# Optimization experiments

Measured on AMD Instinct MI355X. Metric: run time of the kernel, lower is better.

Reference implementation:

```python
import jax, jax.numpy as jnp
import numpy as np
from jax import lax

D_MODEL = 1024
N_HEADS = 16
HEAD_DIM = D_MODEL // N_HEADS
B, S = 4, 2048
EPS = 1e-5


def setup_inputs() -> dict:
    key = jax.random.key(0)
    ks = jax.random.split(key, 8)
    sc = 1.0 / np.sqrt(D_MODEL)
    return {
        "x": jax.random.normal(ks[0], (B, S, D_MODEL), dtype=jnp.float32),
        "Wq": jax.random.normal(ks[1], (D_MODEL, D_MODEL), dtype=jnp.float32) * sc,
        "Wk": jax.random.normal(ks[2], (D_MODEL, D_MODEL), dtype=jnp.float32) * sc,
        "Wv": jax.random.normal(ks[3], (D_MODEL, D_MODEL), dtype=jnp.float32) * sc,
        "Wa": jax.random.normal(ks[4], (D_MODEL, N_HEADS), dtype=jnp.float32) * sc,
        "ba": jnp.zeros((N_HEADS,), dtype=jnp.float32),
        "Wb": jax.random.normal(ks[5], (D_MODEL, N_HEADS), dtype=jnp.float32) * sc,
        "bb": jnp.zeros((N_HEADS,), dtype=jnp.float32),
        "Wg": jax.random.normal(ks[6], (D_MODEL, D_MODEL), dtype=jnp.float32) * sc,
        "Wo": jax.random.normal(ks[7], (D_MODEL, D_MODEL), dtype=jnp.float32) * sc,
        "g_norm": jnp.ones((D_MODEL,), dtype=jnp.float32),
    }


def _l2_normalize(v, eps=1e-12):
    # F.normalize(dim=-1) in float32
    v32 = v.astype(jnp.float32)
    n = jnp.sqrt(jnp.sum(v32 * v32, axis=-1, keepdims=True))
    return (v32 / jnp.maximum(n, eps)).astype(v.dtype)


def _rmsnorm(x, w):
    x32 = x.astype(jnp.float32)
    rms = lax.rsqrt(jnp.mean(x32 * x32, axis=-1, keepdims=True) + EPS)
    return (x32 * rms).astype(x.dtype) * w


def reference(x, Wq, Wk, Wv, Wa, ba, Wb, bb, Wg, Wo, g_norm):
    batch, seq_len, d_model = x.shape
    H, hd = N_HEADS, HEAD_DIM
    residual_input = x

    # projections -> [B, S, H, hd]
    q = (x @ Wq).reshape(batch, seq_len, H, hd)
    k = (x @ Wk).reshape(batch, seq_len, H, hd)
    v = (x @ Wv).reshape(batch, seq_len, H, hd)
    q = _l2_normalize(q)
    k = _l2_normalize(k)

    alpha = jax.nn.sigmoid(x @ Wa + ba)  # [B, S, H]
    beta = jax.nn.sigmoid(x @ Wb + bb)   # [B, S, H]

    # time-major for scan: [S, B, H, ...]
    qt = jnp.moveaxis(q, 1, 0)
    kt = jnp.moveaxis(k, 1, 0)
    vt = jnp.moveaxis(v, 1, 0)
    at = jnp.moveaxis(alpha, 1, 0)
    bt = jnp.moveaxis(beta, 1, 0)

    state0 = jnp.zeros((batch, H, hd, hd), dtype=x.dtype)

    def step(state, inp):
        q_t, k_t, v_t, a_t, b_t = inp  # [B,H,hd], [B,H]
        pred = jnp.einsum('bhde,bhd->bhe', state, k_t)
        error = v_t - pred
        update = jnp.einsum('bhe,bhd->bhde', b_t[..., None] * error, k_t)
        state = a_t[..., None, None] * state + update
        out = jnp.einsum('bhde,bhd->bhe', state, q_t)
        return state, out

    _, ys = lax.scan(step, state0, (qt, kt, vt, at, bt))  # ys: [S,B,H,hd]
    y = jnp.moveaxis(ys, 0, 1).reshape(batch, seq_len, d_model)

    gate = jax.nn.silu(residual_input @ Wg)
    y = _rmsnorm(y, g_norm) * gate
    return y @ Wo


if __name__ == "__main__":
    out = reference(**setup_inputs())
    print(out.shape)
```

## Files before the change

### kernel.cpp

```cpp
#include <hip/hip_runtime.h>
#include <hip/hip_bf16.h>
#include <math.h>

typedef __attribute__((ext_vector_type(8))) short bf16x8s;
typedef __attribute__((ext_vector_type(4))) float f32x4;

#define SEQ 2048
#define NTOK 8192
#define NQKV 3200

static __device__ __forceinline__ float bf2f(unsigned short u) {
  union { unsigned int i; float f; } c; c.i = ((unsigned int)u) << 16; return c.f;
}
static __device__ __forceinline__ unsigned short f2bf(float f) {
  union { float f; unsigned int i; } c; c.f = f;
  unsigned int x = c.i;
  return (unsigned short)((x + 0x7FFFu + ((x >> 16) & 1u)) >> 16);
}

static __device__ __forceinline__ float red16(float x) {
  union { float f; int i; } c, d;
  c.f = x; d.i = __builtin_amdgcn_update_dpp(0, c.i, 0xB1, 0xF, 0xF, true); x += d.f;
  c.f = x; d.i = __builtin_amdgcn_update_dpp(0, c.i, 0x4E, 0xF, 0xF, true); x += d.f;
  c.f = x; d.i = __builtin_amdgcn_update_dpp(0, c.i, 0x141, 0xF, 0xF, true); x += d.f;
  c.f = x; d.i = __builtin_amdgcn_update_dpp(0, c.i, 0x140, 0xF, 0xF, true); x += d.f;
  return x;
}

__global__ __launch_bounds__(256) void castx_k(const float* __restrict__ in,
                                               unsigned short* __restrict__ out, int n4) {
  int i = blockIdx.x * 256 + threadIdx.x;
  if (i >= n4) return;
  float4 v = ((const float4*)in)[i];
  ushort4 o;
  o.x = f2bf(v.x); o.y = f2bf(v.y); o.z = f2bf(v.z); o.w = f2bf(v.w);
  ((ushort4*)out)[i] = o;
}

__global__ void transpose_k(const float* __restrict__ in,
                            unsigned short* __restrict__ out, int R, int C) {
  __shared__ unsigned short tile[32][33];
  int c0 = blockIdx.x * 32, r0 = blockIdx.y * 32;
  int tx = threadIdx.x, ty = threadIdx.y;
  for (int i = ty; i < 32; i += 8)
    tile[i][tx] = f2bf(in[(size_t)(r0 + i) * C + c0 + tx]);
  __syncthreads();
  for (int i = ty; i < 32; i += 8)
    out[(size_t)(c0 + i) * R + r0 + tx] = tile[tx][i];
}

__global__ void build_wabT(const float* __restrict__ Wa,
                           const float* __restrict__ Wb,
                           unsigned short* __restrict__ rows) {
  int i = blockIdx.x * 256 + threadIdx.x;
  int j = i >> 10, k = i & 1023;
  float v = 0.f;
  if (j < 16) v = Wa[k * 16 + j];
  else if (j < 32) v = Wb[k * 16 + (j - 16)];
  rows[(size_t)j * 1024 + k] = f2bf(v);
}

template<int MODE>
__global__ __launch_bounds__(256) void gemm_bt(const unsigned short* __restrict__ A,
                                               const unsigned short* __restrict__ Bt,
                                               void* __restrict__ Cv,
                                               int M, int N, int K,
                                               const float* __restrict__ ba,
                                               const float* __restrict__ bbp,
                                               float* __restrict__ alphaF,
                                               float* __restrict__ betaF) {
  __shared__ __align__(16) unsigned short As[128 * 32];
  __shared__ __align__(16) unsigned short Bs[128 * 32];
  int tiles_n = N >> 7;
  int tm = blockIdx.x / tiles_n, tn = blockIdx.x % tiles_n;
  int m0 = tm << 7, n0 = tn << 7;
  int tid = threadIdx.x;
  int wave = tid >> 6, lane = tid & 63;
  int wm = wave >> 1, wn = wave & 1;
  int r = lane & 15, qd = lane >> 4;
  int lr = lane >> 2, lc = lane & 3;

  f32x4 acc[4][4];
#pragma unroll
  for (int mi = 0; mi < 4; mi++)
#pragma unroll
    for (int ni = 0; ni < 4; ni++) acc[mi][ni] = (f32x4){0.f, 0.f, 0.f, 0.f};

  for (int k0 = 0; k0 < K; k0 += 32) {
#pragma unroll
    for (int gi = 0; gi < 2; ++gi) {
      int g = wave + gi * 4;
      int row = g * 16 + lr;
      const unsigned short* ga = A + (size_t)(m0 + row) * K + k0 + lc * 8;
      const unsigned short* gb = Bt + (size_t)(n0 + row) * K + k0 + lc * 8;
      __builtin_amdgcn_global_load_lds(
          (const __attribute__((address_space(1))) unsigned int*)ga,
          (__attribute__((address_space(3))) unsigned int*)(As + g * 512 + lane * 8),
          16, 0, 0);
      __builtin_amdgcn_global_load_lds(
          (const __attribute__((address_space(1))) unsigned int*)gb,
          (__attribute__((address_space(3))) unsigned int*)(Bs + g * 512 + lane * 8),
          16, 0, 0);
    }
    __syncthreads();
    bf16x8s af[4], bfr[4];
#pragma unroll
    for (int mi = 0; mi < 4; mi++)
      af[mi] = *(const bf16x8s*)&As[(wm * 64 + mi * 16 + r) * 32 + qd * 8];
#pragma unroll
    for (int ni = 0; ni < 4; ni++)
      bfr[ni] = *(const bf16x8s*)&Bs[(wn * 64 + ni * 16 + r) * 32 + qd * 8];
#pragma unroll
    for (int mi = 0; mi < 4; mi++)
#pragma unroll
      for (int ni = 0; ni < 4; ni++)
        acc[mi][ni] = __builtin_amdgcn_mfma_f32_16x16x32_bf16(af[mi], bfr[ni], acc[mi][ni], 0, 0, 0);
    __syncthreads();
  }

  bool qk = (MODE == 2) && (n0 < 2048);
#pragma unroll
  for (int mi = 0; mi < 4; mi++) {
    f32x4 sc = (f32x4){1.f, 1.f, 1.f, 1.f};
    if (qk) {
      f32x4 ss = acc[mi][0] * acc[mi][0] + acc[mi][1] * acc[mi][1]
               + acc[mi][2] * acc[mi][2] + acc[mi][3] * acc[mi][3];
#pragma unroll
      for (int cc = 0; cc < 4; cc++) {
        float s = red16(ss[cc]);
        sc[cc] = 1.f / fmaxf(sqrtf(s), 1e-12f);
      }
    }
#pragma unroll
    for (int ni = 0; ni < 4; ni++)
#pragma unroll
      for (int reg = 0; reg < 4; reg++) {
        int m = m0 + wm * 64 + mi * 16 + qd * 4 + reg;
        int n = n0 + wn * 64 + ni * 16 + r;
        float a = acc[mi][ni][reg];
        if (MODE == 0) ((unsigned short*)Cv)[(size_t)m * N + n] = f2bf(a);
        else if (MODE == 1) ((float*)Cv)[(size_t)m * N + n] = a;
        else {
          if (qk) a *= sc[reg];
          if (n < 3072) ((unsigned short*)Cv)[(size_t)m * 3072 + n] = f2bf(a);
          else if (n < 3104) {
            int j = n - 3072;
            float bias = (j < 16) ? ba[j] : bbp[j - 16];
            float s = 1.f / (1.f + expf(-(a + bias)));
            if (j < 16) alphaF[(size_t)m * 16 + j] = s;
            else        betaF[(size_t)m * 16 + (j - 16)] = s;
          }
        }
      }
  }
}

#define D_OFF_STHI 0
#define D_OFF_STLO 8192
#define D_OFF_K    16384
#define D_OFF_Q    24576
#define D_OFF_V    32768
#define D_OFF_KT   40960
#define D_OFF_MT   45056
#define D_OFF_GBF  53248
#define D_OFF_CTHI 57344
#define D_OFF_CTLO 67584
#define D_OFF_W    77824
#define D_OFF_U    86016
#define D_OFF_AB   102400
#define D_LDS_SIZE 104512

static __device__ __forceinline__ float rdlane(float v, int i) {
  return __int_as_float(__builtin_amdgcn_readlane(__float_as_int(v), i));
}

__global__ __launch_bounds__(512, 2) void dscan_k(const unsigned short* __restrict__ qkv,
                                                  const float* __restrict__ alphaF,
                                                  const float* __restrict__ betaF,
                                                  unsigned short* __restrict__ y) {
  extern __shared__ char smem[];
  const int bh = blockIdx.x;
  const int b = bh >> 4, h = bh & 15;
  const int tid = threadIdx.x, wid = tid >> 6, lane = tid & 63;
  const int r = lane & 15, qd = lane >> 4;

  float* abf = (float*)(smem + D_OFF_AB);

  auto stage_jobs = [&](int cn) {
    int buf = cn & 1;
    int tok0 = b * SEQ + cn * 32;
    int row = lane >> 3, s8 = lane & 7;
    int sx = ((s8 ^ (row & 7)) * 8);
    {
      int p = (wid < 4) ? wid : wid - 4;
      int colbase = (wid < 4) ? (1024 + h * 64) : (h * 64);
      int off = (wid < 4) ? D_OFF_K : D_OFF_Q;
      const unsigned short* src = qkv + (size_t)(tok0 + p * 8 + row) * 3072 + colbase + sx;
      unsigned short* dst = (unsigned short*)(smem + off + buf * 4096 + p * 1024) + lane * 8;
      __builtin_amdgcn_global_load_lds(
          (const __attribute__((address_space(1))) unsigned int*)src,
          (__attribute__((address_space(3))) unsigned int*)dst, 16, 0, 0);
    }
    if (wid < 4) {
      int p = wid;
      const unsigned short* src = qkv + (size_t)(tok0 + p * 8 + row) * 3072 + 2048 + h * 64 + sx;
      unsigned short* dst = (unsigned short*)(smem + D_OFF_V + buf * 4096 + p * 1024) + lane * 8;
      __builtin_amdgcn_global_load_lds(
          (const __attribute__((address_space(1))) unsigned int*)src,
          (__attribute__((address_space(3))) unsigned int*)dst, 16, 0, 0);
    }
  };

  auto ab_compute = [&](int cn) {
    int t = lane & 31;
    int tok = b * SEQ + cn * 32 + t;
    float av = alphaF[(size_t)tok * 16 + h];
    float bv = betaF[(size_t)tok * 16 + h];
    float p = av;
#pragma unroll
    for (int s = 1; s < 32; s <<= 1) {
      float o = __shfl_up(p, s, 32);
      if ((lane & 31) >= s) p *= o;
    }
    float ep = __shfl_up(p, 1, 32);
    if ((lane & 31) == 0) ep = 1.f;
    float* ap = abf + (cn & 3) * 132;
    if (lane < 32) {
      ap[0 + t] = ep;
      ap[32 + t] = p;
      ap[64 + t] = 1.0f / p;
      if (t == 31) ap[128] = p;
    } else {
      ap[96 + t] = bv;
    }
  };

  auto gram_do = [&](int cn) {
    if (wid < 3 || wid > 6) return;
    int buf = cn & 1;
    const char* Kn = smem + D_OFF_K + buf * 4096;
    const char* Qn = smem + D_OFF_Q + buf * 4096;
    const float* ap = abf + (cn & 3) * 132;
    bool kk = (wid <= 4);
    int g0 = (kk ? (wid - 3) : (wid - 5)) * 2;
#pragma unroll
    for (int j = 0; j < 2; ++j) {
      int g = g0 + j, gi = g >> 1, gt = g & 1;
      f32x4 acc = (f32x4){0.f, 0.f, 0.f, 0.f};
#pragma unroll
      for (int ks = 0; ks < 2; ++ks) {
        int o = ks * 64 + qd * 16;
        bf16x8s af = *(const bf16x8s*)(Kn + (gi * 16 + r) * 128 + (o ^ ((r & 7) << 4)));
        bf16x8s bf = kk
            ? *(const bf16x8s*)(Kn + (gt * 16 + r) * 128 + (o ^ ((r & 7) << 4)))
            : *(const bf16x8s*)(Qn + (gt * 16 + r) * 128 + (o ^ ((r & 7) << 4)));
        acc = __builtin_amdgcn_mfma_f32_16x16x32_bf16(af, bf, acc, 0, 0, 0);
      }
      int tl = gt * 16 + r;
      f32x4 ei4 = *(const f32x4*)&ap[64 + gi * 16 + qd * 4];
      if (kk) {
        float bt = ap[96 + tl], ept = ap[0 + tl];
        float* Mtp = (float*)(smem + D_OFF_MT + buf * 4096);
#pragma unroll
        for (int reg = 0; reg < 4; ++reg) {
          int i = gi * 16 + qd * 4 + reg;
          Mtp[i * 32 + tl] = (i < tl) ? bt * ept * ei4[reg] * acc[reg] : 0.f;
        }
      } else {
        float et = ap[32 + tl];
        unsigned short* Gp = (unsigned short*)(smem + D_OFF_GBF + buf * 2048);
#pragma unroll
        for (int reg = 0; reg < 4; ++reg) {
          int i = gi * 16 + qd * 4 + reg;
          float v = (i <= tl) ? et * ei4[reg] * acc[reg] : 0.f;
          Gp[tl * 32 + i] = f2bf(v);
        }
      }
    }
  };

  float sreg[8];
#pragma unroll
  for (int i = 0; i < 8; ++i) sreg[i] = 0.f;

  {
    uint4 z = (uint4){0u, 0u, 0u, 0u};
    *(uint4*)(smem + D_OFF_STHI + tid * 16) = z;
    *(uint4*)(smem + D_OFF_STLO + tid * 16) = z;
  }
  stage_jobs(0);
  if (wid == 0) ab_compute(0);
  else if (wid == 1) ab_compute(1);
  __syncthreads();
  gram_do(0);
  __syncthreads();

  const char* SThi = smem + D_OFF_STHI;
  const char* STlo = smem + D_OFF_STLO;

  for (int c = 0; c < 64; ++c) {
    const int cbuf = c & 1, cs = c & 3;
    if (c + 1 < 64) stage_jobs(c + 1);
    {
      int tt = wid >> 2, te = wid & 3;
      const char* Kc = smem + D_OFF_K + cbuf * 4096;
      f32x4 acc = (f32x4){0.f, 0.f, 0.f, 0.f};
#pragma unroll
      for (int ks = 0; ks < 2; ++ks) {
        int o = ks * 64 + qd * 16;
        bf16x8s af = *(const bf16x8s*)(Kc + (tt * 16 + r) * 128 + (o ^ ((r & 7) << 4)));
        bf16x8s bhv = *(const bf16x8s*)(SThi + (te * 16 + r) * 128 + (o ^ ((r & 7) << 4)));
        bf16x8s blv = *(const bf16x8s*)(STlo + (te * 16 + r) * 128 + (o ^ ((r & 7) << 4)));
        acc = __builtin_amdgcn_mfma_f32_16x16x32_bf16(af, bhv, acc, 0, 0, 0);
        acc = __builtin_amdgcn_mfma_f32_16x16x32_bf16(af, blv, acc, 0, 0, 0);
      }
      float* Wp = (float*)(smem + D_OFF_W);
#pragma unroll
      for (int reg = 0; reg < 4; ++reg)
        Wp[(tt * 16 + qd * 4 + reg) * 64 + te * 16 + r] = acc[reg];
    }
    if (c >= 1) {
      int cc = c - 1, buf = cc & 1;
      int ty = wid >> 2, te = wid & 3;
      const char* Gp = smem + D_OFF_GBF + buf * 2048;
      bf16x8s af = *(const bf16x8s*)(Gp + (ty * 16 + r) * 64 + qd * 16);
      bf16x8s bhv = *(const bf16x8s*)(smem + D_OFF_CTHI + buf * 5120 + (te * 16 + r) * 80 + qd * 16);
      bf16x8s blv = *(const bf16x8s*)(smem + D_OFF_CTLO + buf * 5120 + (te * 16 + r) * 80 + qd * 16);
      f32x4 acc = (f32x4){0.f, 0.f, 0.f, 0.f};
      acc = __builtin_amdgcn_mfma_f32_16x16x32_bf16(af, bhv, acc, 0, 0, 0);
      acc = __builtin_amdgcn_mfma_f32_16x16x32_bf16(af, blv, acc, 0, 0, 0);
      const float* Up = (const float*)(smem + D_OFF_U + buf * 8192);
      f32x4 e4 = *(const f32x4*)&abf[(cc & 3) * 132 + 32 + ty * 16 + qd * 4];
#pragma unroll
      for (int reg = 0; reg < 4; ++reg) {
        int t = ty * 16 + qd * 4 + reg, e = te * 16 + r;
        float yv = fmaf(e4[reg], Up[t * 64 + e], acc[reg]);
        y[(size_t)(b * SEQ + cc * 32 + t) * 1024 + h * 64 + e] = f2bf(yv);
      }
    }
    __syncthreads();

    if (wid == 0) {
      const float* Wp = (const float*)(smem + D_OFF_W);
      const char* Vb = smem + D_OFF_V + cbuf * 4096;
      const float* ap = abf + cs * 132;
      float vb = ap[96 + (lane & 31)];
      float vep = ap[0 + (lane & 31)];
      float d_[32], r_[32];
#pragma unroll
      for (int i = 0; i < 32; ++i) r_[i] = 0.f;
#pragma unroll
      for (int i = 0; i < 32; ++i) {
        float w = Wp[i * 64 + lane];
        unsigned short vx = *(const unsigned short*)(Vb + (i * 128 + ((lane * 2) ^ ((i & 7) << 4))));
        d_[i] = rdlane(vb, i) * fmaf(-rdlane(vep, i), w, bf2f(vx));
      }
      const float* Mtp = (const float*)(smem + D_OFF_MT + cbuf * 4096);
#pragma unroll
      for (int i = 0; i < 32; ++i) {
        float cv = d_[i] - r_[i];
        d_[i] = cv;
#pragma unroll
        for (int cb4 = 0; cb4 < 8; ++cb4) {
          if (cb4 * 4 + 3 > i) {
            f32x4 m4 = *(const f32x4*)&Mtp[i * 32 + cb4 * 4];
            r_[cb4 * 4 + 0] = fmaf(m4[0], cv, r_[cb4 * 4 + 0]);
            r_[cb4 * 4 + 1] = fmaf(m4[1], cv, r_[cb4 * 4 + 1]);
            r_[cb4 * 4 + 2] = fmaf(m4[2], cv, r_[cb4 * 4 + 2]);
            r_[cb4 * 4 + 3] = fmaf(m4[3], cv, r_[cb4 * 4 + 3]);
          }
        }
      }
      unsigned int ph[16], pl[16];
#pragma unroll
      for (int j = 0; j < 16; ++j) {
        unsigned short h0 = f2bf(d_[2 * j]), h1 = f2bf(d_[2 * j + 1]);
        ph[j] = (unsigned int)h0 | ((unsigned int)h1 << 16);
        float l0 = d_[2 * j] - bf2f(h0), l1 = d_[2 * j + 1] - bf2f(h1);
        pl[j] = (unsigned int)f2bf(l0) | ((unsigned int)f2bf(l1) << 16);
      }
      char* Ch = smem + D_OFF_CTHI + cbuf * 5120 + lane * 80;
      char* Cl = smem + D_OFF_CTLO + cbuf * 5120 + lane * 80;
#pragma unroll
      for (int k = 0; k < 4; ++k) {
        *(uint4*)(Ch + k * 16) = (uint4){ph[4 * k], ph[4 * k + 1], ph[4 * k + 2], ph[4 * k + 3]};
        *(uint4*)(Cl + k * 16) = (uint4){pl[4 * k], pl[4 * k + 1], pl[4 * k + 2], pl[4 * k + 3]};
      }
    } else {
      if (wid <= 4) {
        const char* Qc = smem + D_OFF_Q + cbuf * 4096;
        float* Up = (float*)(smem + D_OFF_U + cbuf * 8192);
#pragma unroll
        for (int j = 0; j < 2; ++j) {
          int u = (wid - 1) * 2 + j, tu = u >> 2, te = u & 3;
          f32x4 acc = (f32x4){0.f, 0.f, 0.f, 0.f};
#pragma unroll
          for (int ks = 0; ks < 2; ++ks) {
            int o = ks * 64 + qd * 16;
            bf16x8s af = *(const bf16x8s*)(Qc + (tu * 16 + r) * 128 + (o ^ ((r & 7) << 4)));
            bf16x8s bhv = *(const bf16x8s*)(SThi + (te * 16 + r) * 128 + (o ^ ((r & 7) << 4)));
            bf16x8s blv = *(const bf16x8s*)(STlo + (te * 16 + r) * 128 + (o ^ ((r & 7) << 4)));
            acc = __builtin_amdgcn_mfma_f32_16x16x32_bf16(af, bhv, acc, 0, 0, 0);
            acc = __builtin_amdgcn_mfma_f32_16x16x32_bf16(af, blv, acc, 0, 0, 0);
          }
#pragma unroll
          for (int reg = 0; reg < 4; ++reg)
            Up[(tu * 16 + qd * 4 + reg) * 64 + te * 16 + r] = acc[reg];
        }
      }
      if (c + 1 < 64) gram_do(c + 1);
      if (wid == 7) {
        const float* ap = abf + cs * 132;
        float vei = ap[64 + (lane & 31)];
        float e31 = ap[128];
        const char* Kc = smem + D_OFF_K + cbuf * 4096;
        unsigned short* KT = (unsigned short*)(smem + D_OFF_KT);
        unsigned int pk[16];
#pragma unroll
        for (int i = 0; i < 32; ++i) {
          unsigned short kv = *(const unsigned short*)(Kc + (i * 128 + ((lane * 2) ^ ((i & 7) << 4))));
          float f = bf2f(kv) * (e31 * rdlane(vei, i));
          unsigned short o = f2bf(f);
          if (i & 1) pk[i >> 1] |= ((unsigned int)o << 16);
          else       pk[i >> 1] = o;
        }
#pragma unroll
        for (int k = 0; k < 4; ++k)
          *(uint4*)((char*)KT + lane * 64 + k * 16) =
              (uint4){pk[4 * k], pk[4 * k + 1], pk[4 * k + 2], pk[4 * k + 3]};
      }
      if (wid == 2 && c + 2 < 64) ab_compute(c + 2);
    }
    __syncthreads();

    {
      float e31 = abf[cs * 132 + 128];
      const char* KT = smem + D_OFF_KT;
#pragma unroll
      for (int j = 0; j < 2; ++j) {
        int s = wid * 2 + j, td = s >> 2, te = s & 3;
        bf16x8s af = *(const bf16x8s*)(KT + (td * 16 + r) * 64 + qd * 16);
        bf16x8s bhv = *(const bf16x8s*)(smem + D_OFF_CTHI + cbuf * 5120 + (te * 16 + r) * 80 + qd * 16);
        bf16x8s blv = *(const bf16x8s*)(smem + D_OFF_CTLO + cbuf * 5120 + (te * 16 + r) * 80 + qd * 16);
        f32x4 acc = (f32x4){0.f, 0.f, 0.f, 0.f};
        acc = __builtin_amdgcn_mfma_f32_16x16x32_bf16(af, bhv, acc, 0, 0, 0);
        acc = __builtin_amdgcn_mfma_f32_16x16x32_bf16(af, blv, acc, 0, 0, 0);
#pragma unroll
        for (int reg = 0; reg < 4; ++reg) {
          int d = td * 16 + qd * 4 + reg, e = te * 16 + r;
          float sv = fmaf(e31, sreg[j * 4 + reg], acc[reg]);
          sreg[j * 4 + reg] = sv;
          unsigned short hi = f2bf(sv);
          float lo = sv - bf2f(hi);
          *(unsigned short*)(smem + D_OFF_STHI + e * 128 + ((d * 2) ^ ((e & 7) << 4))) = hi;
          *(unsigned short*)(smem + D_OFF_STLO + e * 128 + ((d * 2) ^ ((e & 7) << 4))) = f2bf(lo);
        }
      }
    }
    __syncthreads();
  }

  {
    int cc = 63, buf = cc & 1;
    int ty = wid >> 2, te = wid & 3;
    const char* Gp = smem + D_OFF_GBF + buf * 2048;
    bf16x8s af = *(const bf16x8s*)(Gp + (ty * 16 + r) * 64 + qd * 16);
    bf16x8s bhv = *(const bf16x8s*)(smem + D_OFF_CTHI + buf * 5120 + (te * 16 + r) * 80 + qd * 16);
    bf16x8s blv = *(const bf16x8s*)(smem + D_OFF_CTLO + buf * 5120 + (te * 16 + r) * 80 + qd * 16);
    f32x4 acc = (f32x4){0.f, 0.f, 0.f, 0.f};
    acc = __builtin_amdgcn_mfma_f32_16x16x32_bf16(af, bhv, acc, 0, 0, 0);
    acc = __builtin_amdgcn_mfma_f32_16x16x32_bf16(af, blv, acc, 0, 0, 0);
    const float* Up = (const float*)(smem + D_OFF_U + buf * 8192);
    f32x4 e4 = *(const f32x4*)&abf[(cc & 3) * 132 + 32 + ty * 16 + qd * 4];
#pragma unroll
    for (int reg = 0; reg < 4; ++reg) {
      int t = ty * 16 + qd * 4 + reg, e = te * 16 + r;
      float yv = fmaf(e4[reg], Up[t * 64 + e], acc[reg]);
      y[(size_t)(b * SEQ + cc * 32 + t) * 1024 + h * 64 + e] = f2bf(yv);
    }
  }
}

__global__ __launch_bounds__(256) void rmsgate_k(const unsigned short* __restrict__ y,
                                                 const unsigned short* __restrict__ gl,
                                                 const float* __restrict__ gnorm,
                                                 unsigned short* __restrict__ z) {
  __shared__ float red[4];
  int row = blockIdx.x, tid = threadIdx.x;
  size_t base = (size_t)row * 1024 + tid * 4;
  uint2 yv = *(const uint2*)&y[base];
  float f0 = bf2f((unsigned short)(yv.x & 0xffff)), f1 = bf2f((unsigned short)(yv.x >> 16));
  float f2 = bf2f((unsigned short)(yv.y & 0xffff)), f3 = bf2f((unsigned short)(yv.y >> 16));
  float ss = f0 * f0 + f1 * f1 + f2 * f2 + f3 * f3;
#pragma unroll
  for (int s = 1; s < 64; s <<= 1) ss += __shfl_xor(ss, s);
  if ((tid & 63) == 0) red[tid >> 6] = ss;
  __syncthreads();
  ss = red[0] + red[1] + red[2] + red[3];
  float rms = rsqrtf(ss * (1.0f / 1024.0f) + 1e-5f);
  uint2 gv = *(const uint2*)&gl[base];
  float4 gn = *(const float4*)&gnorm[tid * 4];
  float g[4] = {bf2f((unsigned short)(gv.x & 0xffff)), bf2f((unsigned short)(gv.x >> 16)),
                bf2f((unsigned short)(gv.y & 0xffff)), bf2f((unsigned short)(gv.y >> 16))};
  float gnv[4] = {gn.x, gn.y, gn.z, gn.w};
  float fv[4] = {f0, f1, f2, f3};
  unsigned short o[4];
#pragma unroll
  for (int jj = 0; jj < 4; jj++) {
    float gate = g[jj] / (1.f + expf(-g[jj]));
    o[jj] = f2bf(fv[jj] * rms * gnv[jj] * gate);
  }
  uint2 ov;
  ov.x = (unsigned int)o[0] | ((unsigned int)o[1] << 16);
  ov.y = (unsigned int)o[2] | ((unsigned int)o[3] << 16);
  *(uint2*)&z[base] = ov;
}

extern "C" void kernel_launch(void* const* d_in, const int* in_sizes, int n_in,
                              void* d_out, int out_size, void* d_ws, size_t ws_size,
                              hipStream_t stream) {
  const float* x     = (const float*)d_in[0];
  const float* Wq    = (const float*)d_in[1];
  const float* Wk    = (const float*)d_in[2];
  const float* Wv    = (const float*)d_in[3];
  const float* Wa    = (const float*)d_in[4];
  const float* ba    = (const float*)d_in[5];
  const float* Wb    = (const float*)d_in[6];
  const float* bb    = (const float*)d_in[7];
  const float* Wg    = (const float*)d_in[8];
  const float* Wo    = (const float*)d_in[9];
  const float* gnorm = (const float*)d_in[10];
  float* out = (float*)d_out;

  unsigned short* xbf    = (unsigned short*)d_ws;
  unsigned short* Bt_qkv = xbf + (size_t)NTOK * 1024;
  unsigned short* Bt_g   = Bt_qkv + (size_t)NQKV * 1024;
  unsigned short* Bt_o   = Bt_g + (size_t)1024 * 1024;
  unsigned short* qkv    = Bt_o + (size_t)1024 * 1024;
  unsigned short* gatelin= qkv + (size_t)NTOK * 3072;
  unsigned short* ybuf   = gatelin + (size_t)NTOK * 1024;
  float* alphaF          = (float*)(ybuf + (size_t)NTOK * 1024);
  float* betaF           = alphaF + (size_t)NTOK * 16;
  unsigned short* zbuf   = xbf;

  static int dscan_inited = 0;
  if (!dscan_inited) {
    hipFuncSetAttribute((const void*)dscan_k,
                        hipFuncAttributeMaxDynamicSharedMemorySize, D_LDS_SIZE);
    dscan_inited = 1;
  }

  castx_k<<<NTOK * 1024 / 4 / 256, 256, 0, stream>>>(x, xbf, NTOK * 1024 / 4);
  dim3 tb(32, 8);
  transpose_k<<<dim3(32, 32), tb, 0, stream>>>(Wq, Bt_qkv, 1024, 1024);
  transpose_k<<<dim3(32, 32), tb, 0, stream>>>(Wk, Bt_qkv + (size_t)1024 * 1024, 1024, 1024);
  transpose_k<<<dim3(32, 32), tb, 0, stream>>>(Wv, Bt_qkv + (size_t)2048 * 1024, 1024, 1024);
  transpose_k<<<dim3(32, 32), tb, 0, stream>>>(Wg, Bt_g, 1024, 1024);
  transpose_k<<<dim3(32, 32), tb, 0, stream>>>(Wo, Bt_o, 1024, 1024);
  build_wabT<<<512, 256, 0, stream>>>(Wa, Wb, Bt_qkv + (size_t)3072 * 1024);

  gemm_bt<2><<<(NTOK / 128) * (NQKV / 128), 256, 0, stream>>>(
      xbf, Bt_qkv, qkv, NTOK, NQKV, 1024, ba, bb, alphaF, betaF);
  gemm_bt<0><<<(NTOK / 128) * (1024 / 128), 256, 0, stream>>>(
      xbf, Bt_g, gatelin, NTOK, 1024, 1024, nullptr, nullptr, nullptr, nullptr);
  dscan_k<<<64, 512, D_LDS_SIZE, stream>>>(qkv, alphaF, betaF, ybuf);
  rmsgate_k<<<NTOK, 256, 0, stream>>>(ybuf, gatelin, gnorm, zbuf);
  gemm_bt<1><<<(NTOK / 128) * (1024 / 128), 256, 0, stream>>>(
      zbuf, Bt_o, out, NTOK, 1024, 1024, nullptr, nullptr, nullptr, nullptr);
}
```

Measured before the change: 538.3 us.

## Split chunked delta-rule scan into parallel prep, serial combine, and parallel output kernels

Replaces the single 64-block sequential scan kernel with three kernels. The first computes per-chunk intra-chunk quantities (WY-style corrections, gram matrices, scaled keys) across 4096 blocks. The second does only the serial inter-chunk state recurrence and writes state snapshots. The third computes outputs in parallel across 2048 blocks. The aim is to move most work off the 64-block critical path, at the cost of large workspace traffic and extra launches. The path is gated on workspace size, and a gram_do prefetch call is also added to the old scan loop.

```diff
diff --git a/kernel.cpp b/kernel.cpp
--- a/kernel.cpp
+++ b/kernel.cpp
@@ -8,6 +8,7 @@
 #define SEQ 2048
 #define NTOK 8192
 #define NQKV 3200
+#define NUNIT 4096
 
 static __device__ __forceinline__ float bf2f(unsigned short u) {
   union { unsigned int i; float f; } c; c.i = ((unsigned int)u) << 16; return c.f;
@@ -26,6 +27,17 @@
   c.f = x; d.i = __builtin_amdgcn_update_dpp(0, c.i, 0x140, 0xF, 0xF, true); x += d.f;
   return x;
 }
+
+static __device__ __forceinline__ float rdlane(float v, int i) {
+  return __int_as_float(__builtin_amdgcn_readlane(__float_as_int(v), i));
+}
+
+#define GLD16(SRC, DST) __builtin_amdgcn_global_load_lds( \
+    (const __attribute__((address_space(1))) unsigned int*)(SRC), \
+    (__attribute__((address_space(3))) unsigned int*)(DST), 16, 0, 0)
+#define GLD4(SRC, DST) __builtin_amdgcn_global_load_lds( \
+    (const __attribute__((address_space(1))) unsigned int*)(SRC), \
+    (__attribute__((address_space(3))) unsigned int*)(DST), 4, 0, 0)
 
 __global__ __launch_bounds__(256) void castx_k(const float* __restrict__ in,
                                                unsigned short* __restrict__ out, int n4) {
@@ -93,14 +105,8 @@
       int row = g * 16 + lr;
       const unsigned short* ga = A + (size_t)(m0 + row) * K + k0 + lc * 8;
       const unsigned short* gb = Bt + (size_t)(n0 + row) * K + k0 + lc * 8;
-      __builtin_amdgcn_global_load_lds(
-          (const __attribute__((address_space(1))) unsigned int*)ga,
-          (__attribute__((address_space(3))) unsigned int*)(As + g * 512 + lane * 8),
-          16, 0, 0);
-      __builtin_amdgcn_global_load_lds(
-          (const __attribute__((address_space(1))) unsigned int*)gb,
-          (__attribute__((address_space(3))) unsigned int*)(Bs + g * 512 + lane * 8),
-          16, 0, 0);
+      GLD16(ga, As + g * 512 + lane * 8);
+      GLD16(gb, Bs + g * 512 + lane * 8);
     }
     __syncthreads();
     bf16x8s af[4], bfr[4];
@@ -170,10 +176,6 @@
 #define D_OFF_AB   102400
 #define D_LDS_SIZE 104512
 
-static __device__ __forceinline__ float rdlane(float v, int i) {
-  return __int_as_float(__builtin_amdgcn_readlane(__float_as_int(v), i));
-}
-
 __global__ __launch_bounds__(512, 2) void dscan_k(const unsigned short* __restrict__ qkv,
                                                   const float* __restrict__ alphaF,
                                                   const float* __restrict__ betaF,
@@ -197,17 +199,13 @@
       int off = (wid < 4) ? D_OFF_K : D_OFF_Q;
       const unsigned short* src = qkv + (size_t)(tok0 + p * 8 + row) * 3072 + colbase + sx;
       unsigned short* dst = (unsigned short*)(smem + off + buf * 4096 + p * 1024) + lane * 8;
-      __builtin_amdgcn_global_load_lds(
-          (const __attribute__((address_space(1))) unsigned int*)src,
-          (__attribute__((address_space(3))) unsigned int*)dst, 16, 0, 0);
+      GLD16(src, dst);
     }
     if (wid < 4) {
       int p = wid;
       const unsigned short* src = qkv + (size_t)(tok0 + p * 8 + row) * 3072 + 2048 + h * 64 + sx;
       unsigned short* dst = (unsigned short*)(smem + D_OFF_V + buf * 4096 + p * 1024) + lane * 8;
-      __builtin_amdgcn_global_load_lds(
-          (const __attribute__((address_space(1))) unsigned int*)src,
-          (__attribute__((address_space(3))) unsigned int*)dst, 16, 0, 0);
+      GLD16(src, dst);
     }
   };
 
@@ -457,6 +455,7 @@
         }
       }
     }
+    if (c + 1 < 64) gram_do(c + 1);
     __syncthreads();
   }
 
@@ -477,6 +476,454 @@
       int t = ty * 16 + qd * 4 + reg, e = te * 16 + r;
       float yv = fmaf(e4[reg], Up[t * 64 + e], acc[reg]);
       y[(size_t)(b * SEQ + cc * 32 + t) * 1024 + h * 64 + e] = f2bf(yv);
+    }
+  }
+}
+
+#define AK   0
+#define AQ   4096
+#define AV   8192
+#define AMT  12288
+#define AGS  16896
+#define AKP  19456
+#define AAB  24576
+#define ASZ  25120
+
+__global__ __launch_bounds__(256) void aprep_k(const unsigned short* __restrict__ qkv,
+                                               const float* __restrict__ alphaF,
+                                               const float* __restrict__ betaF,
+                                               unsigned char* __restrict__ RbHi,
+                                               unsigned char* __restrict__ RbLo,
+                                               unsigned char* __restrict__ Kpg,
+                                               unsigned char* __restrict__ Gg,
+                                               float* __restrict__ wg,
+                                               float* __restrict__ eing) {
+  __shared__ __align__(16) char smA[ASZ];
+  const int u = blockIdx.x;
+  const int bh = u >> 6, c = u & 63;
+  const int b = bh >> 4, h = bh & 15;
+  const int tid = threadIdx.x, wid = tid >> 6, lane = tid & 63;
+  const int r = lane & 15, qd = lane >> 4;
+  float* ab = (float*)(smA + AAB);
+
+  {
+    int tok0 = b * SEQ + c * 32;
+    int row = lane >> 3, s8 = lane & 7;
+    int sx = ((s8 ^ (row & 7)) * 8);
+    const unsigned short* base = qkv + (size_t)(tok0 + wid * 8 + row) * 3072 + h * 64 + sx;
+    GLD16(base + 1024, smA + AK + wid * 1024 + lane * 16);
+    GLD16(base,        smA + AQ + wid * 1024 + lane * 16);
+    GLD16(base + 2048, smA + AV + wid * 1024 + lane * 16);
+  }
+  if (wid == 0) {
+    int t = lane & 31;
+    int tok = b * SEQ + c * 32 + t;
+    float av = alphaF[(size_t)tok * 16 + h];
+    float bv = betaF[(size_t)tok * 16 + h];
+    float p = av;
+#pragma unroll
+    for (int s = 1; s < 32; s <<= 1) {
+      float o = __shfl_up(p, s, 32);
+      if ((lane & 31) >= s) p *= o;
+    }
+    float ep = __shfl_up(p, 1, 32);
+    if ((lane & 31) == 0) ep = 1.f;
+    if (lane < 32) {
+      ab[0 + t] = ep;
+      ab[32 + t] = p;
+      ab[64 + t] = 1.0f / p;
+      if (t == 31) ab[128] = p;
+    } else {
+      ab[96 + t] = bv;
+    }
+  }
+  __syncthreads();
+
+  const int sw = ((r & 7) << 4);
+  if (wid < 2) {
+    int gi = wid;
+    float* Mtp = (float*)(smA + AMT);
+    f32x4 ei4 = *(const f32x4*)&ab[64 + gi * 16 + qd * 4];
+#pragma unroll
+    for (int gt = 0; gt < 2; ++gt) {
+      f32x4 acc = (f32x4){0.f, 0.f, 0.f, 0.f};
+#pragma unroll
+      for (int ks = 0; ks < 2; ++ks) {
+        int o = ks * 64 + qd * 16;
+        bf16x8s af = *(const bf16x8s*)(smA + AK + (gi * 16 + r) * 128 + (o ^ sw));
+        bf16x8s bf = *(const bf16x8s*)(smA + AK + (gt * 16 + r) * 128 + (o ^ sw));
+        acc = __builtin_amdgcn_mfma_f32_16x16x32_bf16(af, bf, acc, 0, 0, 0);
+      }
+      int tl = gt * 16 + r;
+      float bep = ab[96 + tl] * ab[0 + tl];
+#pragma unroll
+      for (int reg = 0; reg < 4; ++reg) {
+        int i = gi * 16 + qd * 4 + reg;
+        Mtp[i * 36 + tl] = (i < tl) ? bep * ei4[reg] * acc[reg] : 0.f;
+      }
+    }
+  } else {
+    int gi = wid - 2;
+    unsigned short* Gp = (unsigned short*)(smA + AGS);
+    f32x4 ei4 = *(const f32x4*)&ab[64 + gi * 16 + qd * 4];
+#pragma unroll
+    for (int gt = 0; gt < 2; ++gt) {
+      f32x4 acc = (f32x4){0.f, 0.f, 0.f, 0.f};
+#pragma unroll
+      for (int ks = 0; ks < 2; ++ks) {
+        int o = ks * 64 + qd * 16;
+        bf16x8s af = *(const bf16x8s*)(smA + AK + (gi * 16 + r) * 128 + (o ^ sw));
+        bf16x8s bf = *(const bf16x8s*)(smA + AQ + (gt * 16 + r) * 128 + (o ^ sw));
+        acc = __builtin_amdgcn_mfma_f32_16x16x32_bf16(af, bf, acc, 0, 0, 0);
+      }
+      int tl = gt * 16 + r;
+      float et = ab[32 + tl];
+#pragma unroll
+      for (int reg = 0; reg < 4; ++reg) {
+        int i = gi * 16 + qd * 4 + reg;
+        float v = (i <= tl) ? et * ei4[reg] * acc[reg] : 0.f;
+        Gp[tl * 40 + i] = f2bf(v);
+      }
+    }
+    {
+      int i0 = (wid - 2) * 16;
+      float e31 = ab[128];
+#pragma unroll
+      for (int ii = 0; ii < 16; ++ii) {
+        int i = i0 + ii;
+        unsigned short kv = *(const unsigned short*)(smA + AK + i * 128 + ((lane * 2) ^ ((i & 7) << 4)));
+        float f = bf2f(kv) * (e31 * ab[64 + i]);
+        *(unsigned short*)(smA + AKP + lane * 64 + ((i * 2) ^ ((lane & 3) << 4))) = f2bf(f);
+      }
+    }
+  }
+  __syncthreads();
+
+  if (wid < 2) {
+    float d_[32], r_[32];
+#pragma unroll
+    for (int i = 0; i < 32; ++i) r_[i] = 0.f;
+#pragma unroll
+    for (int i = 0; i < 32; ++i) {
+      unsigned short xv;
+      if (wid == 0) xv = *(const unsigned short*)(smA + AK + i * 128 + ((lane * 2) ^ ((i & 7) << 4)));
+      else          xv = *(const unsigned short*)(smA + AV + i * 128 + ((lane * 2) ^ ((i & 7) << 4)));
+      float scv = (wid == 0) ? ab[96 + i] * ab[0 + i] : ab[96 + i];
+      d_[i] = scv * bf2f(xv);
+    }
+    const float* Mtp = (const float*)(smA + AMT);
+#pragma unroll
+    for (int i = 0; i < 32; ++i) {
+      float cv = d_[i] - r_[i];
+      d_[i] = cv;
+#pragma unroll
+      for (int cb4 = 0; cb4 < 8; ++cb4) {
+        if (cb4 * 4 + 3 > i) {
+          f32x4 m4 = *(const f32x4*)&Mtp[i * 36 + cb4 * 4];
+          r_[cb4 * 4 + 0] = fmaf(m4[0], cv, r_[cb4 * 4 + 0]);
+          r_[cb4 * 4 + 1] = fmaf(m4[1], cv, r_[cb4 * 4 + 1]);
+          r_[cb4 * 4 + 2] = fmaf(m4[2], cv, r_[cb4 * 4 + 2]);
+          r_[cb4 * 4 + 3] = fmaf(m4[3], cv, r_[cb4 * 4 + 3]);
+        }
+      }
+    }
+    if (wid == 0) {
+      size_t ub = (size_t)u * 4096;
+#pragma unroll
+      for (int t = 0; t < 32; ++t) {
+        unsigned short hi = f2bf(d_[t]);
+        float lo = d_[t] - bf2f(hi);
+        int off = t * 128 + ((lane * 2) ^ ((t & 7) << 4));
+        *(unsigned short*)(RbHi + ub + off) = hi;
+        *(unsigned short*)(RbLo + ub + off) = f2bf(lo);
+      }
+    } else {
+      float* wp = wg + (size_t)u * 2048;
+#pragma unroll
+      for (int t = 0; t < 32; ++t) wp[t * 64 + lane] = d_[t];
+    }
+  } else if (wid == 2) {
+    const char* s = smA + AGS + lane * 40;
+    unsigned char* dG = Gg + (size_t)u * 2560 + lane * 40;
+#pragma unroll
+    for (int k2 = 0; k2 < 5; ++k2)
+      *(uint2*)(dG + k2 * 8) = *(const uint2*)(s + k2 * 8);
+    if (lane < 32) eing[(size_t)u * 64 + lane] = ab[32 + lane];
+    if (lane == 32) eing[(size_t)u * 64 + 32] = ab[128];
+  } else {
+    const char* s = smA + AKP;
+    unsigned char* dK = Kpg + (size_t)u * 4096;
+#pragma unroll
+    for (int k2 = 0; k2 < 4; ++k2)
+      *(uint4*)(dK + lane * 64 + k2 * 16) = *(const uint4*)(s + lane * 64 + k2 * 16);
+  }
+}
+
+#define BSH  0
+#define BSL  8192
+#define BRH  16384
+#define BRL  24576
+#define BKP  32768
+#define BW   40960
+#define BCTH 57344
+#define BCTL 61440
+#define BSZ  65536
+
+__global__ __launch_bounds__(256) void bcomb_k(const unsigned char* __restrict__ RbHi,
+                                               const unsigned char* __restrict__ RbLo,
+                                               const unsigned char* __restrict__ Kpg,
+                                               float* __restrict__ wcg,
+                                               const float* __restrict__ eing,
+                                               unsigned char* __restrict__ Sing) {
+  extern __shared__ char smB[];
+  const int bh = blockIdx.x;
+  const int u_base = bh * 64;
+  const int tid = threadIdx.x, wid = tid >> 6, lane = tid & 63;
+  const int r = lane & 15, qd = lane >> 4;
+  const int sw7 = ((r & 7) << 4), sw3 = ((r & 3) << 4);
+
+  auto stageB = [&](int cn, int buf) {
+    int u = u_base + cn;
+    for (int j = wid; j < 20; j += 4) {
+      const unsigned char* src; char* dst;
+      if (j < 4)       { src = RbHi + (size_t)u * 4096 + j * 1024;       dst = smB + BRH + buf * 4096 + j * 1024; }
+      else if (j < 8)  { src = RbLo + (size_t)u * 4096 + (j - 4) * 1024; dst = smB + BRL + buf * 4096 + (j - 4) * 1024; }
+      else if (j < 12) { src = Kpg + (size_t)u * 4096 + (j - 8) * 1024;  dst = smB + BKP + buf * 4096 + (j - 8) * 1024; }
+      else             { src = (const unsigned char*)wcg + (size_t)u * 8192 + (j - 12) * 1024;
+                         dst = smB + BW + buf * 8192 + (j - 12) * 1024; }
+      GLD16(src + lane * 16, dst + lane * 16);
+    }
+  };
+
+#pragma unroll
+  for (int k = 0; k < 4; ++k)
+    *(uint4*)(smB + tid * 64 + k * 16) = (uint4){0u, 0u, 0u, 0u};
+  float sreg[16];
+#pragma unroll
+  for (int i = 0; i < 16; ++i) sreg[i] = 0.f;
+
+  stageB(0, 0);
+  float e31c = eing[(size_t)u_base * 64 + 32];
+  __syncthreads();
+
+  for (int c = 0; c < 64; ++c) {
+    const int buf = c & 1;
+    const int u = u_base + c;
+    float e31n = 0.f;
+    if (c + 1 < 64) {
+      stageB(c + 1, buf ^ 1);
+      e31n = eing[(size_t)(u + 1) * 64 + 32];
+    }
+    if (!(c & 1)) {
+#pragma unroll
+      for (int k = 0; k < 4; ++k)
+        *(uint4*)(Sing + (size_t)(u >> 1) * 16384 + k * 4096 + tid * 16) =
+            *(const uint4*)(smB + k * 4096 + tid * 16);
+    }
+    f32x4 accP[2];
+#pragma unroll
+    for (int tt = 0; tt < 2; ++tt) {
+      accP[tt] = (f32x4){0.f, 0.f, 0.f, 0.f};
+#pragma unroll
+      for (int ks = 0; ks < 2; ++ks) {
+        int o = ks * 64 + qd * 16;
+        bf16x8s sh = *(const bf16x8s*)(smB + BSH + (wid * 16 + r) * 128 + (o ^ sw7));
+        bf16x8s sl = *(const bf16x8s*)(smB + BSL + (wid * 16 + r) * 128 + (o ^ sw7));
+        bf16x8s rh = *(const bf16x8s*)(smB + BRH + buf * 4096 + (tt * 16 + r) * 128 + (o ^ sw7));
+        bf16x8s rl = *(const bf16x8s*)(smB + BRL + buf * 4096 + (tt * 16 + r) * 128 + (o ^ sw7));
+        accP[tt] = __builtin_amdgcn_mfma_f32_16x16x32_bf16(rh, sh, accP[tt], 0, 0, 0);
+        accP[tt] = __builtin_amdgcn_mfma_f32_16x16x32_bf16(rh, sl, accP[tt], 0, 0, 0);
+        accP[tt] = __builtin_amdgcn_mfma_f32_16x16x32_bf16(rl, sh, accP[tt], 0, 0, 0);
+      }
+    }
+    {
+      const float* wp = (const float*)(smB + BW + buf * 8192);
+#pragma unroll
+      for (int tt = 0; tt < 2; ++tt)
+#pragma unroll
+        for (int reg = 0; reg < 4; ++reg) {
+          int t = tt * 16 + qd * 4 + reg, e = wid * 16 + r;
+          float cv = wp[t * 64 + e] - accP[tt][reg];
+          unsigned short hi = f2bf(cv);
+          int off = e * 64 + ((t * 2) ^ ((e & 3) << 4));
+          *(unsigned short*)(smB + BCTH + off) = hi;
+          *(unsigned short*)(smB + BCTL + off) = f2bf(cv - bf2f(hi));
+        }
+    }
+    __syncthreads();
+    *(uint4*)((unsigned char*)wcg + (size_t)u * 8192 + tid * 16) =
+        *(const uint4*)(smB + BCTH + tid * 16);
+    *(uint4*)((unsigned char*)wcg + (size_t)u * 8192 + 4096 + tid * 16) =
+        *(const uint4*)(smB + BCTL + tid * 16);
+#pragma unroll
+    for (int j = 0; j < 4; ++j) {
+      f32x4 acc = (f32x4){0.f, 0.f, 0.f, 0.f};
+      bf16x8s af = *(const bf16x8s*)(smB + BKP + buf * 4096 + (wid * 16 + r) * 64 + ((qd * 16) ^ sw3));
+      bf16x8s ch = *(const bf16x8s*)(smB + BCTH + (j * 16 + r) * 64 + ((qd * 16) ^ sw3));
+      bf16x8s cl = *(const bf16x8s*)(smB + BCTL + (j * 16 + r) * 64 + ((qd * 16) ^ sw3));
+      acc = __builtin_amdgcn_mfma_f32_16x16x32_bf16(af, ch, acc, 0, 0, 0);
+      acc = __builtin_amdgcn_mfma_f32_16x16x32_bf16(af, cl, acc, 0, 0, 0);
+#pragma unroll
+      for (int reg = 0; reg < 4; ++reg) {
+        int d = wid * 16 + qd * 4 + reg, e = j * 16 + r;
+        float sv = fmaf(e31c, sreg[j * 4 + reg], acc[reg]);
+        sreg[j * 4 + reg] = sv;
+        unsigned short hi = f2bf(sv);
+        int off = e * 128 + ((d * 2) ^ ((e & 7) << 4));
+        *(unsigned short*)(smB + BSH + off) = hi;
+        *(unsigned short*)(smB + BSL + off) = f2bf(sv - bf2f(hi));
+      }
+    }
+    e31c = e31n;
+    __syncthreads();
+  }
+}
+
+#define XSH  0
+#define XSL  8192
+#define XQ   16384
+#define XC   24576
+#define XG   40960
+#define XKP  46080
+#define XSZ  50176
+
+__global__ __launch_bounds__(256) void cout2_k(const unsigned short* __restrict__ qkv,
+                                               const float* __restrict__ wcg,
+                                               const unsigned char* __restrict__ Gg,
+                                               const unsigned char* __restrict__ Kpg,
+                                               const float* __restrict__ eing,
+                                               const unsigned char* __restrict__ Sing,
+                                               unsigned short* __restrict__ y) {
+  __shared__ __align__(16) char smC[XSZ];
+  const int p = blockIdx.x;
+  const int bh = p >> 5, pr = p & 31;
+  const int b = bh >> 4, h = bh & 15;
+  const int u0 = bh * 64 + pr * 2;
+  const int tid = threadIdx.x, wid = tid >> 6, lane = tid & 63;
+  const int r = lane & 15, qd = lane >> 4;
+  const int sw7 = ((r & 7) << 4), sw3 = ((r & 3) << 4);
+  const int tok0 = b * SEQ + pr * 64;
+
+  for (int j = wid; j < 44; j += 4) {
+    if (j < 16) {
+      GLD16(Sing + (size_t)(u0 >> 1) * 16384 + j * 1024 + lane * 16,
+            smC + XSH + j * 1024 + lane * 16);
+    } else if (j < 24) {
+      int q = (j - 16) >> 2, pt = (j - 16) & 3;
+      int row = lane >> 3, s8 = lane & 7;
+      int sx = ((s8 ^ (row & 7)) * 8);
+      const unsigned short* src = qkv + (size_t)(tok0 + q * 32 + pt * 8 + row) * 3072 + h * 64 + sx;
+      GLD16(src, smC + XQ + q * 4096 + pt * 1024 + lane * 16);
+    } else if (j < 40) {
+      int q = (j - 24) >> 3, pt = (j - 24) & 7;
+      GLD16((const unsigned char*)wcg + (size_t)(u0 + q) * 8192 + pt * 1024 + lane * 16,
+            smC + XC + q * 8192 + pt * 1024 + lane * 16);
+    } else {
+      GLD16(Kpg + (size_t)u0 * 4096 + (j - 40) * 1024 + lane * 16,
+            smC + XKP + (j - 40) * 1024 + lane * 16);
+    }
+  }
+  if (wid < 2) {
+    const unsigned char* src = Gg + (size_t)(u0 + wid) * 2560;
+    char* dst = smC + XG + wid * 2560;
+    GLD16(src + lane * 16, dst + lane * 16);
+    GLD16(src + 1024 + lane * 16, dst + 1024 + lane * 16);
+    GLD4(src + 2048 + lane * 4, dst + 2048 + lane * 4);
+    GLD4(src + 2304 + lane * 4, dst + 2304 + lane * 4);
+  }
+  __syncthreads();
+
+  f32x4 accS[4];
+#pragma unroll
+  for (int half = 0; half < 1; ++half) {
+    f32x4 accU[2], accG[2];
+#pragma unroll
+    for (int tt = 0; tt < 2; ++tt) {
+      accU[tt] = (f32x4){0.f, 0.f, 0.f, 0.f};
+#pragma unroll
+      for (int ks = 0; ks < 2; ++ks) {
+        int o = ks * 64 + qd * 16;
+        bf16x8s sh = *(const bf16x8s*)(smC + XSH + (wid * 16 + r) * 128 + (o ^ sw7));
+        bf16x8s sl = *(const bf16x8s*)(smC + XSL + (wid * 16 + r) * 128 + (o ^ sw7));
+        bf16x8s qa = *(const bf16x8s*)(smC + XQ + (tt * 16 + r) * 128 + (o ^ sw7));
+        accU[tt] = __builtin_amdgcn_mfma_f32_16x16x32_bf16(qa, sh, accU[tt], 0, 0, 0);
+        accU[tt] = __builtin_amdgcn_mfma_f32_16x16x32_bf16(qa, sl, accU[tt], 0, 0, 0);
+      }
+      bf16x8s ga = *(const bf16x8s*)(smC + XG + (tt * 16 + r) * 80 + qd * 16);
+      bf16x8s ch = *(const bf16x8s*)(smC + XC + (wid * 16 + r) * 64 + ((qd * 16) ^ sw3));
+      bf16x8s cl = *(const bf16x8s*)(smC + XC + 4096 + (wid * 16 + r) * 64 + ((qd * 16) ^ sw3));
+      accG[tt] = (f32x4){0.f, 0.f, 0.f, 0.f};
+      accG[tt] = __builtin_amdgcn_mfma_f32_16x16x32_bf16(ga, ch, accG[tt], 0, 0, 0);
+      accG[tt] = __builtin_amdgcn_mfma_f32_16x16x32_bf16(ga, cl, accG[tt], 0, 0, 0);
+    }
+#pragma unroll
+    for (int tt = 0; tt < 2; ++tt) {
+      f32x4 e4 = *(const f32x4*)&eing[(size_t)u0 * 64 + tt * 16 + qd * 4];
+#pragma unroll
+      for (int reg = 0; reg < 4; ++reg) {
+        int t = tt * 16 + qd * 4 + reg, e = wid * 16 + r;
+        y[(size_t)(tok0 + t) * 1024 + h * 64 + e] =
+            f2bf(fmaf(e4[reg], accU[tt][reg], accG[tt][reg]));
+      }
+    }
+#pragma unroll
+    for (int j = 0; j < 4; ++j) {
+      accS[j] = (f32x4){0.f, 0.f, 0.f, 0.f};
+      bf16x8s af = *(const bf16x8s*)(smC + XKP + (wid * 16 + r) * 64 + ((qd * 16) ^ sw3));
+      bf16x8s ch = *(const bf16x8s*)(smC + XC + (j * 16 + r) * 64 + ((qd * 16) ^ sw3));
+      bf16x8s cl = *(const bf16x8s*)(smC + XC + 4096 + (j * 16 + r) * 64 + ((qd * 16) ^ sw3));
+      accS[j] = __builtin_amdgcn_mfma_f32_16x16x32_bf16(af, ch, accS[j], 0, 0, 0);
+      accS[j] = __builtin_amdgcn_mfma_f32_16x16x32_bf16(af, cl, accS[j], 0, 0, 0);
+    }
+  }
+  __syncthreads();
+  {
+    float e31 = eing[(size_t)u0 * 64 + 32];
+#pragma unroll
+    for (int j = 0; j < 4; ++j)
+#pragma unroll
+      for (int reg = 0; reg < 4; ++reg) {
+        int d = wid * 16 + qd * 4 + reg, e = j * 16 + r;
+        int off = e * 128 + ((d * 2) ^ ((e & 7) << 4));
+        float sA = bf2f(*(const unsigned short*)(smC + XSH + off)) +
+                   bf2f(*(const unsigned short*)(smC + XSL + off));
+        float sv = fmaf(e31, sA, accS[j][reg]);
+        unsigned short hi = f2bf(sv);
+        *(unsigned short*)(smC + XSH + off) = hi;
+        *(unsigned short*)(smC + XSL + off) = f2bf(sv - bf2f(hi));
+      }
+  }
+  __syncthreads();
+  {
+    f32x4 accU[2], accG[2];
+#pragma unroll
+    for (int tt = 0; tt < 2; ++tt) {
+      accU[tt] = (f32x4){0.f, 0.f, 0.f, 0.f};
+#pragma unroll
+      for (int ks = 0; ks < 2; ++ks) {
+        int o = ks * 64 + qd * 16;
+        bf16x8s sh = *(const bf16x8s*)(smC + XSH + (wid * 16 + r) * 128 + (o ^ sw7));
+        bf16x8s sl = *(const bf16x8s*)(smC + XSL + (wid * 16 + r) * 128 + (o ^ sw7));
+        bf16x8s qa = *(const bf16x8s*)(smC + XQ + 4096 + (tt * 16 + r) * 128 + (o ^ sw7));
+        accU[tt] = __builtin_amdgcn_mfma_f32_16x16x32_bf16(qa, sh, accU[tt], 0, 0, 0);
+        accU[tt] = __builtin_amdgcn_mfma_f32_16x16x32_bf16(qa, sl, accU[tt], 0, 0, 0);
+      }
+      bf16x8s ga = *(const bf16x8s*)(smC + XG + 2560 + (tt * 16 + r) * 80 + qd * 16);
+      bf16x8s ch = *(const bf16x8s*)(smC + XC + 8192 + (wid * 16 + r) * 64 + ((qd * 16) ^ sw3));
+      bf16x8s cl = *(const bf16x8s*)(smC + XC + 8192 + 4096 + (wid * 16 + r) * 64 + ((qd * 16) ^ sw3));
+      accG[tt] = (f32x4){0.f, 0.f, 0.f, 0.f};
+      accG[tt] = __builtin_amdgcn_mfma_f32_16x16x32_bf16(ga, ch, accG[tt], 0, 0, 0);
+      accG[tt] = __builtin_amdgcn_mfma_f32_16x16x32_bf16(ga, cl, accG[tt], 0, 0, 0);
+    }
+#pragma unroll
+    for (int tt = 0; tt < 2; ++tt) {
+      f32x4 e4 = *(const f32x4*)&eing[(size_t)(u0 + 1) * 64 + tt * 16 + qd * 4];
+#pragma unroll
+      for (int reg = 0; reg < 4; ++reg) {
+        int t = tt * 16 + qd * 4 + reg, e = wid * 16 + r;
+        y[(size_t)(tok0 + 32 + t) * 1024 + h * 64 + e] =
+            f2bf(fmaf(e4[reg], accU[tt][reg], accG[tt][reg]));
+      }
     }
   }
 }
@@ -543,11 +990,23 @@
   float* betaF           = alphaF + (size_t)NTOK * 16;
   unsigned short* zbuf   = xbf;
 
-  static int dscan_inited = 0;
-  if (!dscan_inited) {
+  unsigned char* RbHi = (unsigned char*)xbf;
+  unsigned char* RbLo = (unsigned char*)ybuf;
+  float* eing         = (float*)Bt_qkv;
+  unsigned char* Kpg  = (unsigned char*)(betaF + (size_t)NTOK * 16);
+  unsigned char* Gg   = Kpg + (size_t)NUNIT * 4096;
+  float* wcg          = (float*)(Gg + (size_t)NUNIT * 2560);
+  unsigned char* Sing = (unsigned char*)wcg + (size_t)NUNIT * 8192;
+  const unsigned long long need_new = 206831616ull;
+  const bool use_new = (ws_size >= need_new);
+
+  static int inited = 0;
+  if (!inited) {
     hipFuncSetAttribute((const void*)dscan_k,
                         hipFuncAttributeMaxDynamicSharedMemorySize, D_LDS_SIZE);
-    dscan_inited = 1;
+    hipFuncSetAttribute((const void*)bcomb_k,
+                        hipFuncAttributeMaxDynamicSharedMemorySize, BSZ);
+    inited = 1;
   }
 
   castx_k<<<NTOK * 1024 / 4 / 256, 256, 0, stream>>>(x, xbf, NTOK * 1024 / 4);
@@ -563,7 +1022,15 @@
       xbf, Bt_qkv, qkv, NTOK, NQKV, 1024, ba, bb, alphaF, betaF);
   gemm_bt<0><<<(NTOK / 128) * (1024 / 128), 256, 0, stream>>>(
       xbf, Bt_g, gatelin, NTOK, 1024, 1024, nullptr, nullptr, nullptr, nullptr);
-  dscan_k<<<64, 512, D_LDS_SIZE, stream>>>(qkv, alphaF, betaF, ybuf);
+
+  if (use_new) {
+    aprep_k<<<NUNIT, 256, 0, stream>>>(qkv, alphaF, betaF, RbHi, RbLo, Kpg, Gg, wcg, eing);
+    bcomb_k<<<64, 256, BSZ, stream>>>(RbHi, RbLo, Kpg, wcg, eing, Sing);
+    cout2_k<<<2048, 256, 0, stream>>>(qkv, wcg, Gg, Kpg, eing, Sing, ybuf);
+  } else {
+    dscan_k<<<64, 512, D_LDS_SIZE, stream>>>(qkv, alphaF, betaF, ybuf);
+  }
+
   rmsgate_k<<<NTOK, 256, 0, stream>>>(ybuf, gatelin, gnorm, zbuf);
   gemm_bt<1><<<(NTOK / 128) * (1024 / 128), 256, 0, stream>>>(
       zbuf, Bt_o, out, NTOK, 1024, 1024, nullptr, nullptr, nullptr, nullptr);
```

Result: faster. 515.4 us (-4.3%).
